# Kernel tuning notes

Hardware: AMD Instinct MI355X
Metric: run time of the kernel (lower is better)

## Reference

```python
import jax, jax.numpy as jnp
import numpy as np

# config (matches init_kwargs)
B, N, C_IN = 2, 16384, 64
NPOINT, NSAMPLE, RADIUS = 2048, 32, 0.8
MLP = [64, 128, 256]
EPS = 1e-5


def _fps(xyz, npoint):
    """Furthest point sampling. xyz: (B,N,3) -> idx (B,npoint) int32."""
    b, n, _ = xyz.shape
    d0 = jnp.sum((xyz - xyz[:, :1, :]) ** 2, -1)  # dist to point 0

    def body(mind, _):
        nxt = jnp.argmax(mind, -1)                       # (B,)
        pt = jnp.take_along_axis(xyz, nxt[:, None, None], 1)  # (B,1,3)
        mind = jnp.minimum(mind, jnp.sum((xyz - pt) ** 2, -1))
        return mind, nxt

    _, idxs = jax.lax.scan(body, d0, None, length=npoint - 1)  # (npoint-1,B)
    idxs = jnp.concatenate([jnp.zeros((1, b), idxs.dtype), idxs], 0)
    return jnp.transpose(idxs).astype(jnp.int32)


def _ball_query(xyz, new_xyz, radius, nsample):
    """First nsample neighbors within radius (pointnet2 semantics: pad with first hit)."""
    n = xyz.shape[1]
    d = jnp.sum((new_xyz[:, :, None, :] - xyz[:, None, :, :]) ** 2, -1)  # (B,np,N)
    mask = d < radius * radius
    # prefer lowest original index among in-range points
    score = jnp.where(mask, -jnp.arange(n, dtype=jnp.float32), -(n + 1.0))
    vals, idxs = jax.lax.top_k(score, nsample)           # (B,np,ns)
    valid = vals > -(n + 0.5)
    idx = jnp.where(valid, idxs, idxs[..., :1])
    cnt = mask.sum(-1)                                    # (B,np)
    return idx.astype(jnp.int32), cnt


def _gather(arr, idx):  # arr (B,N,...), idx (B,...) -> (B,...,...)
    return jax.vmap(lambda a, i: a[i])(arr, idx)


def _bn_eval4(x, g, b):  # (B,C,P,S), eval-mode BN with running mean 0 / var 1
    s = g / jnp.sqrt(1.0 + EPS)
    return x * s[None, :, None, None] + b[None, :, None, None]


def _bn_eval3(x, g, b):  # (B,C,S)
    s = g / jnp.sqrt(1.0 + EPS)
    return x * s[None, :, None] + b[None, :, None]


def setup_inputs() -> dict:
    key = jax.random.key(0)
    ks = jax.random.split(key, 12)
    xyz = jax.random.normal(ks[0], (B, N, 3), jnp.float32)
    features = jax.random.normal(ks[1], (B, C_IN, N), jnp.float32)
    cin = 3 + C_IN
    dims = [cin] + MLP
    inp = {"xyz": xyz, "features": features}
    for li in range(3):
        w = jax.random.normal(ks[2 + li], (dims[li + 1], dims[li]), jnp.float32) / np.sqrt(dims[li])
        inp[f"W{li+1}"] = w
        inp[f"g{li+1}"] = jnp.ones((dims[li + 1],), jnp.float32)
        inp[f"b{li+1}"] = jnp.zeros((dims[li + 1],), jnp.float32)
    npt8, cd, cd8 = NPOINT // 8, MLP[-1], MLP[-1] // 8
    inp["Wq"] = jax.random.normal(ks[5], (npt8, NPOINT), jnp.float32) / np.sqrt(NPOINT)
    inp["gq"] = jnp.ones((npt8,), jnp.float32)
    inp["bq"] = jnp.zeros((npt8,), jnp.float32)
    inp["Wk"] = jax.random.normal(ks[6], (npt8, NPOINT), jnp.float32) / np.sqrt(NPOINT)
    inp["gk"] = jnp.ones((npt8,), jnp.float32)
    inp["bk"] = jnp.zeros((npt8,), jnp.float32)
    inp["We1"] = jax.random.normal(ks[7], (cd8, cd), jnp.float32) / np.sqrt(cd)
    inp["We2"] = jax.random.normal(ks[8], (cd, cd8), jnp.float32) / np.sqrt(cd8)
    inp["alpha"] = jnp.zeros((1,), jnp.float32)  # torch: nn.Parameter(torch.zeros(1))
    return inp


def reference(xyz, features, W1, g1, b1, W2, g2, b2, W3, g3, b3,
              Wq, gq, bq, Wk, gk, bk, We1, We2, alpha):
    # ---- d-FPS sampling (indices are non-differentiable, as in the CUDA op) ----
    xyz_c = jax.lax.stop_gradient(xyz)
    samp = _fps(xyz_c, NPOINT)                       # (B,np)
    new_xyz = _gather(xyz, samp)                     # (B,np,3)
    # ---- ball query + grouping ----
    nn_idx, cnt = _ball_query(xyz_c, jax.lax.stop_gradient(new_xyz), RADIUS, NSAMPLE)
    grouped_xyz = _gather(xyz, nn_idx) - new_xyz[:, :, None, :]        # (B,np,ns,3)
    grouped_feat = _gather(jnp.transpose(features, (0, 2, 1)), nn_idx)  # (B,np,ns,C)
    h = jnp.transpose(jnp.concatenate([grouped_xyz, grouped_feat], -1), (0, 3, 1, 2))  # (B,3+C,np,ns)
    # ---- shared MLP (1x1 conv + BN(eval) + ReLU) ----
    for (w, g, b) in ((W1, g1, b1), (W2, g2, b2), (W3, g3, b3)):
        h = jax.nn.relu(_bn_eval4(jnp.einsum('oi,bips->bops', w, h), g, b))
    h = h * (cnt > 0)[:, None, :, None].astype(h.dtype)  # mask empty balls
    x = jnp.max(h, axis=-1)                               # (B,Cd,np) max-pool over nsample
    # ---- LCEF channel-affinity attention ----
    xh = jnp.transpose(x, (0, 2, 1))                      # (B,np,Cd)
    q = jax.nn.relu(_bn_eval3(jnp.einsum('oi,bis->bos', Wq, xh), gq, bq))  # (B,np/8,Cd)
    k = jax.nn.relu(_bn_eval3(jnp.einsum('oi,bis->bos', Wk, xh), gk, bk))  # (B,np/8,Cd)
    sim = jnp.einsum('bqc,bqd->bcd', k, q)                # (B,Cd,Cd)
    aff = jax.nn.softmax(jnp.max(sim, -1, keepdims=True) - sim, axis=-1)
    s = jnp.max(x, -1)                                    # (B,Cd) squeeze
    e = jax.nn.sigmoid(jnp.einsum('oi,bi->bo', We2, jax.nn.relu(jnp.einsum('oi,bi->bo', We1, s))))
    v = x * e[:, :, None]                                 # excitation
    out = alpha[0] * jnp.einsum('bcd,bdn->bcn', aff, v) + x
    return new_xyz, out
```

## Files before the change

kernel.cpp:

```cpp
#include <hip/hip_runtime.h>
#include <hip/hip_bf16.h>

typedef unsigned short ushort_t;
typedef unsigned int uint_t;
typedef unsigned long long ull_t;

#define B_    2
#define N_    16384
#define NP_   2048
#define NS_   32
#define EPSF  1e-5f

__device__ __forceinline__ float bf2f(ushort_t u) { return __uint_as_float(((uint_t)u) << 16); }

__device__ __forceinline__ int dtflag(const uint_t* g1w) {
  return (g1w[0] == 0x3F803F80u) ? 1 : 0;
}

__device__ __forceinline__ float dist2(float dx, float dy, float dz) {
  return __fadd_rn(__fadd_rn(__fmul_rn(dx, dx), __fmul_rn(dy, dy)), __fmul_rn(dz, dz));
}

template<int CTRL, int RMASK>
__device__ __forceinline__ float dppmax(float x) {
  int m = __builtin_amdgcn_update_dpp(0, __float_as_int(x), CTRL, RMASK, 0xf, true);
  return fmaxf(x, __int_as_float(m));
}
__device__ __forceinline__ float rlanef(float x, int l) {
  return __int_as_float(__builtin_amdgcn_readlane(__float_as_int(x), l));
}

struct CvtTab { const void* src[18]; };
__constant__ int c_psz[18] = {4288, 64, 64, 8192, 128, 128, 32768, 256, 256,
                              524288, 256, 256, 524288, 256, 256, 8192, 8192, 1};
__constant__ int c_poff[18] = {0, 4288, 4352, 4416, 12608, 12736, 12864, 45632, 45888,
                               46144, 570432, 570688, 570944, 1095232, 1095488,
                               1095744, 1103936, 1112128};

__global__ void k_cvt_all(CvtTab tab, float* __restrict__ par) {
  int p = blockIdx.y;
  int n = c_psz[p];
  int i = blockIdx.x * 256 + threadIdx.x;
  if (i >= n) return;
  int f = dtflag((const uint_t*)tab.src[1]);
  float v = f ? bf2f(((const ushort_t*)tab.src[p])[i]) : ((const float*)tab.src[p])[i];
  par[c_poff[p] + i] = v;
}

__global__ void k_wt(const float* __restrict__ W1f, const float* __restrict__ W2f,
                     const float* __restrict__ W3f, float* __restrict__ Wt) {
  int which = blockIdx.y;
  int i = blockIdx.x * 256 + threadIdx.x;
  if (which == 0) {
    if (i >= 4288) return;
    int o = i / 67, k = i - o * 67;
    Wt[k * 64 + o] = W1f[i];
  } else if (which == 1) {
    if (i >= 8192) return;
    int o = i >> 6, k = i & 63;
    Wt[4288 + k * 128 + o] = W2f[i];
  } else {
    if (i >= 32768) return;
    int o = i >> 7, k = i & 127;
    Wt[12480 + k * 256 + o] = W3f[i];
  }
}

__global__ void k_xyz_soa(const void* __restrict__ xyz, const uint_t* __restrict__ g1w,
                          float* __restrict__ X, float* __restrict__ Y, float* __restrict__ Z) {
  int g = blockIdx.x * blockDim.x + threadIdx.x;
  if (g >= B_ * N_) return;
  if (dtflag(g1w)) {
    const ushort_t* p = (const ushort_t*)xyz;
    X[g] = bf2f(p[g * 3 + 0]); Y[g] = bf2f(p[g * 3 + 1]); Z[g] = bf2f(p[g * 3 + 2]);
  } else {
    const float* p = (const float*)xyz;
    X[g] = p[g * 3 + 0]; Y[g] = p[g * 3 + 1]; Z[g] = p[g * 3 + 2];
  }
}

__global__ void k_featT(const void* __restrict__ feat, const uint_t* __restrict__ g1w,
                        float* __restrict__ featF) {
  __shared__ float tile[64 * 65];
  int b = blockIdx.x >> 8, n0 = (blockIdx.x & 255) * 64, t = threadIdx.x;
  int f = dtflag(g1w);
  for (int i = t; i < 4096; i += 256) {
    int c = i >> 6, nn = i & 63;
    size_t src = (size_t)(b * 64 + c) * N_ + n0 + nn;
    tile[c * 65 + nn] = f ? bf2f(((const ushort_t*)feat)[src]) : ((const float*)feat)[src];
  }
  __syncthreads();
  for (int i = t; i < 4096; i += 256) {
    int nn = i >> 6, c = i & 63;
    featF[((size_t)(b * N_ + n0 + nn)) * 64 + c] = tile[c * 65 + nn];
  }
}

__global__ __launch_bounds__(1024)
__attribute__((amdgpu_waves_per_eu(4, 4)))
void k_fps12(const float* __restrict__ X,
             const float* __restrict__ Y,
             const float* __restrict__ Z,
             float* __restrict__ nxf,
             void* __restrict__ outp,
             const uint_t* __restrict__ g1w) {
  __shared__ float sv[16];
  __shared__ float bc[4];
  int b = blockIdx.x, t = threadIdx.x;
  int lane = t & 63, wid = t >> 6;
  int f = dtflag(g1w);
  const float* Xb = X + b * N_;
  const float* Yb = Y + b * N_;
  const float* Zb = Z + b * N_;
  float cx = Xb[0], cy = Yb[0], cz = Zb[0];
  if (t == 0) {
    int base = b * NP_ * 3;
    nxf[base + 0] = cx; nxf[base + 1] = cy; nxf[base + 2] = cz;
    if (f) {
      __hip_bfloat16* o = (__hip_bfloat16*)outp;
      o[base + 0] = __float2bfloat16(cx); o[base + 1] = __float2bfloat16(cy); o[base + 2] = __float2bfloat16(cz);
    } else {
      float* o = (float*)outp;
      o[base + 0] = cx; o[base + 1] = cy; o[base + 2] = cz;
    }
  }
  float x[16], y[16], z[16], md[16];
#pragma unroll
  for (int c = 0; c < 4; c++) {
    float4 xv = ((const float4*)Xb)[(t << 2) + c];
    float4 yv = ((const float4*)Yb)[(t << 2) + c];
    float4 zv = ((const float4*)Zb)[(t << 2) + c];
    x[4 * c + 0] = xv.x; x[4 * c + 1] = xv.y; x[4 * c + 2] = xv.z; x[4 * c + 3] = xv.w;
    y[4 * c + 0] = yv.x; y[4 * c + 1] = yv.y; y[4 * c + 2] = yv.z; y[4 * c + 3] = yv.w;
    z[4 * c + 0] = zv.x; z[4 * c + 1] = zv.y; z[4 * c + 2] = zv.z; z[4 * c + 3] = zv.w;
    md[4 * c + 0] = dist2(xv.x - cx, yv.x - cy, zv.x - cz);
    md[4 * c + 1] = dist2(xv.y - cx, yv.y - cy, zv.y - cz);
    md[4 * c + 2] = dist2(xv.z - cx, yv.z - cy, zv.z - cz);
    md[4 * c + 3] = dist2(xv.w - cx, yv.w - cy, zv.w - cz);
  }
#pragma unroll
  for (int k = 0; k < 16; k++)
    asm volatile("" : "+v"(x[k]), "+v"(y[k]), "+v"(z[k]));

  for (int it = 1; it < NP_; it++) {
    float q0 = fmaxf(fmaxf(md[0], md[1]),   fmaxf(md[2], md[3]));
    float q1 = fmaxf(fmaxf(md[4], md[5]),   fmaxf(md[6], md[7]));
    float q2 = fmaxf(fmaxf(md[8], md[9]),   fmaxf(md[10], md[11]));
    float q3 = fmaxf(fmaxf(md[12], md[13]), fmaxf(md[14], md[15]));
    float lm = fmaxf(fmaxf(q0, q1), fmaxf(q2, q3));
    float v = lm;
    v = dppmax<0x111, 0xf>(v);
    v = dppmax<0x112, 0xf>(v);
    v = dppmax<0x114, 0xf>(v);
    v = dppmax<0x118, 0xf>(v);
    v = dppmax<0x142, 0xa>(v);
    v = dppmax<0x143, 0xc>(v);
    float wm = rlanef(v, 63);
    ull_t m1 = __ballot(lm == wm);
    int wlead = __ffsll((unsigned long long)m1) - 1;
    if (lane == wlead) sv[wid] = wm;
    __syncthreads();
    float pv = sv[lane & 15];
    float q = pv;
    q = dppmax<0x111, 0xf>(q);
    q = dppmax<0x112, 0xf>(q);
    q = dppmax<0x114, 0xf>(q);
    q = dppmax<0x118, 0xf>(q);
    float bm = rlanef(q, 15);
    ull_t m2 = __ballot((lane < 16) && (pv == bm));
    int wwave = __ffsll((unsigned long long)m2) - 1;
    if (wid == wwave && lane == wlead) {
      float wx = x[0], wy = y[0], wz = z[0];
#pragma unroll
      for (int k = 15; k >= 0; k--)
        if (md[k] == lm) { wx = x[k]; wy = y[k]; wz = z[k]; }
      bc[0] = wx; bc[1] = wy; bc[2] = wz;
      int base = (b * NP_ + it) * 3;
      nxf[base + 0] = wx; nxf[base + 1] = wy; nxf[base + 2] = wz;
      if (f) {
        __hip_bfloat16* o = (__hip_bfloat16*)outp;
        o[base + 0] = __float2bfloat16(wx); o[base + 1] = __float2bfloat16(wy); o[base + 2] = __float2bfloat16(wz);
      } else {
        float* o = (float*)outp;
        o[base + 0] = wx; o[base + 1] = wy; o[base + 2] = wz;
      }
    }
    __syncthreads();
    cx = bc[0]; cy = bc[1]; cz = bc[2];
#pragma unroll
    for (int k = 0; k < 16; k++)
      md[k] = fminf(md[k], dist2(x[k] - cx, y[k] - cy, z[k] - cz));
  }
}

__global__ void k_ball(const float* __restrict__ X, const float* __restrict__ Y,
                       const float* __restrict__ Z, const float* __restrict__ nxf,
                       int* __restrict__ nnidx) {
  __shared__ int ibuf[4][NS_];
  int t = threadIdx.x, w = t >> 6, lane = t & 63;
  int cid = blockIdx.x * 4 + w;
  int b = cid >> 11;
  const float* Xb = X + b * N_;
  const float* Yb = Y + b * N_;
  const float* Zb = Z + b * N_;
  float cx = nxf[cid * 3 + 0], cy = nxf[cid * 3 + 1], cz = nxf[cid * 3 + 2];
  int found = 0;
  for (int c = 0; c < N_ / 64; c++) {
    int n = c * 64 + lane;
    float d = dist2(Xb[n] - cx, Yb[n] - cy, Zb[n] - cz);
    bool pred = d < 0.64f;
    ull_t mask = __ballot(pred);
    if (pred) {
      int rank = found + __popcll(mask & ((1ull << lane) - 1ull));
      if (rank < NS_) ibuf[w][rank] = n;
    }
    found += __popcll(mask);
    if (found >= NS_) break;
  }
  __syncthreads();
  if (lane < NS_) {
    int idx = (lane < found) ? ibuf[w][lane] : ibuf[w][0];
    nnidx[cid * NS_ + lane] = idx;
  }
}

__global__ __launch_bounds__(256) void k_mlp(
    const float* __restrict__ featF, const float* __restrict__ X,
    const float* __restrict__ Y, const float* __restrict__ Z,
    const float* __restrict__ nxf, const int* __restrict__ nnidx,
    const float* __restrict__ Wt,
    const float* __restrict__ g1f, const float* __restrict__ b1f,
    const float* __restrict__ g2f, const float* __restrict__ b2f,
    const float* __restrict__ g3f, const float* __restrict__ b3f,
    float* __restrict__ x_nc) {
  __shared__ __align__(16) char smem[33280];
  float* h2f = (float*)smem;
  float* h0f = (float*)(smem + 16384);
  float* h1f = (float*)(smem + 24960);
  int* idxs  = (int*)(smem + 33152);
  const float* Wt1 = Wt;
  const float* Wt2 = Wt + 4288;
  const float* Wt3 = Wt + 12480;

  int t = threadIdx.x;
  int cid = blockIdx.x;
  int b = cid >> 11;
  if (t < 32) idxs[t] = nnidx[cid * NS_ + t];
  __syncthreads();
  float cx = nxf[cid * 3 + 0], cy = nxf[cid * 3 + 1], cz = nxf[cid * 3 + 2];
  if (t < 32) {
    int n = b * N_ + idxs[t];
    h0f[0 * 32 + t] = X[n] - cx;
    h0f[1 * 32 + t] = Y[n] - cy;
    h0f[2 * 32 + t] = Z[n] - cz;
  }
  {
    int s = t >> 3, cg = t & 7;
    const float* fr = featF + ((size_t)(b * N_ + idxs[s])) * 64 + cg * 8;
    float4 a = ((const float4*)fr)[0];
    float4 c2 = ((const float4*)fr)[1];
    int kb = 3 + cg * 8;
    h0f[(kb + 0) * 32 + s] = a.x;  h0f[(kb + 1) * 32 + s] = a.y;
    h0f[(kb + 2) * 32 + s] = a.z;  h0f[(kb + 3) * 32 + s] = a.w;
    h0f[(kb + 4) * 32 + s] = c2.x; h0f[(kb + 5) * 32 + s] = c2.y;
    h0f[(kb + 6) * 32 + s] = c2.z; h0f[(kb + 7) * 32 + s] = c2.w;
  }
  __syncthreads();

  int og = t >> 3, sg = t & 7;
  int s0 = sg * 4;
  {
    int o0 = og * 2;
    float acc[2][4] = {{0, 0, 0, 0}, {0, 0, 0, 0}};
    for (int k = 0; k < 67; k++) {
      float4 h = *(const float4*)(h0f + k * 32 + s0);
      float2 wp = *(const float2*)(Wt1 + k * 64 + o0);
      acc[0][0] = fmaf(wp.x, h.x, acc[0][0]);
      acc[0][1] = fmaf(wp.x, h.y, acc[0][1]);
      acc[0][2] = fmaf(wp.x, h.z, acc[0][2]);
      acc[0][3] = fmaf(wp.x, h.w, acc[0][3]);
      acc[1][0] = fmaf(wp.y, h.x, acc[1][0]);
      acc[1][1] = fmaf(wp.y, h.y, acc[1][1]);
      acc[1][2] = fmaf(wp.y, h.z, acc[1][2]);
      acc[1][3] = fmaf(wp.y, h.w, acc[1][3]);
    }
#pragma unroll
    for (int i2 = 0; i2 < 2; i2++) {
      int o = o0 + i2;
      float sc = g1f[o] / sqrtf(1.0f + EPSF);
      float bb = b1f[o];
      float4 yv;
      yv.x = fmaxf(fmaf(acc[i2][0], sc, bb), 0.0f);
      yv.y = fmaxf(fmaf(acc[i2][1], sc, bb), 0.0f);
      yv.z = fmaxf(fmaf(acc[i2][2], sc, bb), 0.0f);
      yv.w = fmaxf(fmaf(acc[i2][3], sc, bb), 0.0f);
      *(float4*)(h1f + o * 32 + s0) = yv;
    }
  }
  __syncthreads();
  {
    int o0 = og * 4;
    float acc[4][4] = {{0,0,0,0},{0,0,0,0},{0,0,0,0},{0,0,0,0}};
    for (int k = 0; k < 64; k++) {
      float4 h = *(const float4*)(h1f + k * 32 + s0);
      float4 wp = *(const float4*)(Wt2 + k * 128 + o0);
      float w[4] = {wp.x, wp.y, wp.z, wp.w};
#pragma unroll
      for (int i2 = 0; i2 < 4; i2++) {
        acc[i2][0] = fmaf(w[i2], h.x, acc[i2][0]);
        acc[i2][1] = fmaf(w[i2], h.y, acc[i2][1]);
        acc[i2][2] = fmaf(w[i2], h.z, acc[i2][2]);
        acc[i2][3] = fmaf(w[i2], h.w, acc[i2][3]);
      }
    }
#pragma unroll
    for (int i2 = 0; i2 < 4; i2++) {
      int o = o0 + i2;
      float sc = g2f[o] / sqrtf(1.0f + EPSF);
      float bb = b2f[o];
      float4 yv;
      yv.x = fmaxf(fmaf(acc[i2][0], sc, bb), 0.0f);
      yv.y = fmaxf(fmaf(acc[i2][1], sc, bb), 0.0f);
      yv.z = fmaxf(fmaf(acc[i2][2], sc, bb), 0.0f);
      yv.w = fmaxf(fmaf(acc[i2][3], sc, bb), 0.0f);
      *(float4*)(h2f + o * 32 + s0) = yv;
    }
  }
  __syncthreads();
  float acc3[8][4] = {{0,0,0,0},{0,0,0,0},{0,0,0,0},{0,0,0,0},
                      {0,0,0,0},{0,0,0,0},{0,0,0,0},{0,0,0,0}};
  int o0 = og * 8;
  for (int kg = 0; kg < 128; kg++) {
    float4 h = *(const float4*)(h2f + kg * 32 + s0);
    float4 wa = *(const float4*)(Wt3 + kg * 256 + o0);
    float4 wc = *(const float4*)(Wt3 + kg * 256 + o0 + 4);
    float w[8] = {wa.x, wa.y, wa.z, wa.w, wc.x, wc.y, wc.z, wc.w};
#pragma unroll
    for (int i2 = 0; i2 < 8; i2++) {
      acc3[i2][0] = fmaf(w[i2], h.x, acc3[i2][0]);
      acc3[i2][1] = fmaf(w[i2], h.y, acc3[i2][1]);
      acc3[i2][2] = fmaf(w[i2], h.z, acc3[i2][2]);
      acc3[i2][3] = fmaf(w[i2], h.w, acc3[i2][3]);
    }
  }
  float mx[8];
#pragma unroll
  for (int i2 = 0; i2 < 8; i2++) {
    int o = o0 + i2;
    float sc = g3f[o] / sqrtf(1.0f + EPSF);
    float bb = b3f[o];
    float m0 = fmaxf(fmaf(acc3[i2][0], sc, bb), 0.0f);
    float m1 = fmaxf(fmaf(acc3[i2][1], sc, bb), 0.0f);
    float m2 = fmaxf(fmaf(acc3[i2][2], sc, bb), 0.0f);
    float m3 = fmaxf(fmaf(acc3[i2][3], sc, bb), 0.0f);
    mx[i2] = fmaxf(fmaxf(m0, m1), fmaxf(m2, m3));
  }
#pragma unroll
  for (int off = 1; off < 8; off <<= 1) {
#pragma unroll
    for (int i2 = 0; i2 < 8; i2++) mx[i2] = fmaxf(mx[i2], __shfl_xor(mx[i2], off));
  }
  if (sg == 0) {
    float4 a, c;
    a.x = mx[0]; a.y = mx[1]; a.z = mx[2]; a.w = mx[3];
    c.x = mx[4]; c.y = mx[5]; c.z = mx[6]; c.w = mx[7];
    *(float4*)(x_nc + (size_t)cid * 256 + o0) = a;
    *(float4*)(x_nc + (size_t)cid * 256 + o0 + 4) = c;
  }
}

__global__ __launch_bounds__(256) void k_sqmax(const float* __restrict__ x_nc,
                                               float* __restrict__ sqpart) {
  int b = blockIdx.x >> 4, chunk = blockIdx.x & 15, t = threadIdx.x;
  const float* xb = x_nc + (size_t)b * NP_ * 256 + (size_t)chunk * 128 * 256;
  float m = -1e30f;
#pragma unroll 8
  for (int n = 0; n < 128; n++) m = fmaxf(m, xb[(size_t)n * 256 + t]);
  sqpart[(size_t)(b * 16 + chunk) * 256 + t] = m;
}

__global__ __launch_bounds__(256) void k_sqe2(const float* __restrict__ sqpart,
                                              const float* __restrict__ We1f,
                                              const float* __restrict__ We2f,
                                              float* __restrict__ e) {
  __shared__ float ssh[256];
  __shared__ float ush[32];
  int b = blockIdx.x, t = threadIdx.x;
  const float* pp = sqpart + (size_t)b * 16 * 256;
  float m = -1e30f;
#pragma unroll
  for (int c = 0; c < 16; c++) m = fmaxf(m, pp[c * 256 + t]);
  ssh[t] = m;
  __syncthreads();
  if (t < 32) {
    float a = 0.0f;
    for (int i = 0; i < 256; i++) a = fmaf(We1f[t * 256 + i], ssh[i], a);
    ush[t] = fmaxf(a, 0.0f);
  }
  __syncthreads();
  float a = 0.0f;
#pragma unroll
  for (int j = 0; j < 32; j++) a = fmaf(We2f[t * 32 + j], ush[j], a);
  e[b * 256 + t] = 1.0f / (1.0f + expf(-a));
}

__global__ __launch_bounds__(256) void k_qk(const float* __restrict__ x_nc,
                                            const float* __restrict__ Wqf, const float* __restrict__ gqf, const float* __restrict__ bqf,
                                            const float* __restrict__ Wkf, const float* __restrict__ gkf, const float* __restrict__ bkf,
                                            float* __restrict__ qb, float* __restrict__ kb) {
  __shared__ float As[32 * 33];
  __shared__ float Bs[32 * 64];
  int bid = blockIdx.x;
  int b = bid & 1, tq = (bid >> 1) & 1, mt = (bid >> 2) & 7, nt = (bid >> 5) & 3;
  const float* W = tq ? Wkf : Wqf;
  const float* g = tq ? gkf : gqf;
  const float* bb_ = tq ? bkf : bqf;
  float* outp = tq ? kb : qb;
  int t = threadIdx.x;
  int o0 = (t >> 4) * 2, c0 = (t & 15) * 4;
  float acc[2][4] = {{0,0,0,0},{0,0,0,0}};
  for (int k0 = 0; k0 < NP_; k0 += 32) {
    for (int i = t; i < 1024; i += 256) {
      int row = i >> 5, kk = i & 31;
      As[row * 33 + kk] = W[(size_t)(mt * 32 + row) * NP_ + k0 + kk];
    }
    for (int i = t; i < 2048; i += 256) {
      int kk = i >> 6, cc = i & 63;
      Bs[kk * 64 + cc] = x_nc[((size_t)(b * NP_ + k0 + kk)) * 256 + nt * 64 + cc];
    }
    __syncthreads();
    for (int kk = 0; kk < 32; kk++) {
      float4 bv = *(const float4*)(Bs + kk * 64 + c0);
      float a0 = As[(o0 + 0) * 33 + kk];
      float a1 = As[(o0 + 1) * 33 + kk];
      acc[0][0] = fmaf(a0, bv.x, acc[0][0]); acc[0][1] = fmaf(a0, bv.y, acc[0][1]);
      acc[0][2] = fmaf(a0, bv.z, acc[0][2]); acc[0][3] = fmaf(a0, bv.w, acc[0][3]);
      acc[1][0] = fmaf(a1, bv.x, acc[1][0]); acc[1][1] = fmaf(a1, bv.y, acc[1][1]);
      acc[1][2] = fmaf(a1, bv.z, acc[1][2]); acc[1][3] = fmaf(a1, bv.w, acc[1][3]);
    }
    __syncthreads();
  }
#pragma unroll
  for (int i2 = 0; i2 < 2; i2++) {
    int o = mt * 32 + o0 + i2;
    float sc = g[o] / sqrtf(1.0f + EPSF);
    float bv = bb_[o];
    float4 y;
    y.x = fmaxf(fmaf(acc[i2][0], sc, bv), 0.0f);
    y.y = fmaxf(fmaf(acc[i2][1], sc, bv), 0.0f);
    y.z = fmaxf(fmaf(acc[i2][2], sc, bv), 0.0f);
    y.w = fmaxf(fmaf(acc[i2][3], sc, bv), 0.0f);
    *(float4*)(outp + ((size_t)(b * 256 + o)) * 256 + nt * 64 + c0) = y;
  }
}

__global__ __launch_bounds__(256) void k_sim(const float* __restrict__ qb,
                                             const float* __restrict__ kb,
                                             float* __restrict__ sim) {
  __shared__ float As[32 * 64];
  __shared__ float Bs[32 * 64];
  int bid = blockIdx.x;
  int b = bid & 1, ct = (bid >> 1) & 3, dt = (bid >> 3) & 3;
  int t = threadIdx.x;
  int c0 = (t >> 4) * 4, d0 = (t & 15) * 4;
  float acc[4][4] = {{0,0,0,0},{0,0,0,0},{0,0,0,0},{0,0,0,0}};
  for (int k0 = 0; k0 < 256; k0 += 32) {
    for (int i = t; i < 2048; i += 256) {
      int kk = i >> 6, cc = i & 63;
      As[kk * 64 + cc] = kb[((size_t)(b * 256 + k0 + kk)) * 256 + ct * 64 + cc];
      Bs[kk * 64 + cc] = qb[((size_t)(b * 256 + k0 + kk)) * 256 + dt * 64 + cc];
    }
    __syncthreads();
    for (int kk = 0; kk < 32; kk++) {
      float4 av = *(const float4*)(As + kk * 64 + c0);
      float4 bv = *(const float4*)(Bs + kk * 64 + d0);
      acc[0][0] = fmaf(av.x, bv.x, acc[0][0]); acc[0][1] = fmaf(av.x, bv.y, acc[0][1]);
      acc[0][2] = fmaf(av.x, bv.z, acc[0][2]); acc[0][3] = fmaf(av.x, bv.w, acc[0][3]);
      acc[1][0] = fmaf(av.y, bv.x, acc[1][0]); acc[1][1] = fmaf(av.y, bv.y, acc[1][1]);
      acc[1][2] = fmaf(av.y, bv.z, acc[1][2]); acc[1][3] = fmaf(av.y, bv.w, acc[1][3]);
      acc[2][0] = fmaf(av.z, bv.x, acc[2][0]); acc[2][1] = fmaf(av.z, bv.y, acc[2][1]);
      acc[2][2] = fmaf(av.z, bv.z, acc[2][2]); acc[2][3] = fmaf(av.z, bv.w, acc[2][3]);
      acc[3][0] = fmaf(av.w, bv.x, acc[3][0]); acc[3][1] = fmaf(av.w, bv.y, acc[3][1]);
      acc[3][2] = fmaf(av.w, bv.z, acc[3][2]); acc[3][3] = fmaf(av.w, bv.w, acc[3][3]);
    }
    __syncthreads();
  }
#pragma unroll
  for (int i2 = 0; i2 < 4; i2++) {
    *(float4*)(sim + ((size_t)(b * 256 + ct * 64 + c0 + i2)) * 256 + dt * 64 + d0) =
        *(float4*)acc[i2];
  }
}

__global__ void k_aff(const float* __restrict__ sim, float* __restrict__ aff) {
  int t = threadIdx.x, w = t >> 6, lane = t & 63;
  int row = blockIdx.x * 4 + w;
  const float* sr = sim + (size_t)row * 256;
  float4 v = *(const float4*)(sr + lane * 4);
  float mx = fmaxf(fmaxf(v.x, v.y), fmaxf(v.z, v.w));
#pragma unroll
  for (int off = 32; off >= 1; off >>= 1) mx = fmaxf(mx, __shfl_xor(mx, off));
  float4 u;
  u.x = mx - v.x; u.y = mx - v.y; u.z = mx - v.z; u.w = mx - v.w;
  float um = fmaxf(fmaxf(u.x, u.y), fmaxf(u.z, u.w));
#pragma unroll
  for (int off = 32; off >= 1; off >>= 1) um = fmaxf(um, __shfl_xor(um, off));
  float4 p;
  p.x = expf(u.x - um); p.y = expf(u.y - um); p.z = expf(u.z - um); p.w = expf(u.w - um);
  float s = ((p.x + p.y) + (p.z + p.w));
#pragma unroll
  for (int off = 32; off >= 1; off >>= 1) s += __shfl_xor(s, off);
  float4 o;
  o.x = p.x / s; o.y = p.y / s; o.z = p.z / s; o.w = p.w / s;
  *(float4*)(aff + (size_t)row * 256 + lane * 4) = o;
}

__global__ __launch_bounds__(256) void k_out(const float* __restrict__ aff,
                                             const float* __restrict__ x_nc,
                                             const float* __restrict__ e,
                                             const float* __restrict__ alphaf,
                                             void* __restrict__ outp,
                                             const uint_t* __restrict__ g1w) {
  __shared__ float Acs[64 * 33];
  __shared__ float Bs[32 * 65];
  __shared__ float Xs[64 * 65];
  int bid = blockIdx.x;
  int b = bid & 1, ct = (bid >> 1) & 3, nt = bid >> 3;
  int t = threadIdx.x;
  int c0 = (t >> 4) * 4, n0 = (t & 15) * 4;
  float acc[4][4] = {{0,0,0,0},{0,0,0,0},{0,0,0,0},{0,0,0,0}};
  for (int k0 = 0; k0 < 256; k0 += 32) {
    for (int i = t; i < 2048; i += 256) {
      int cc = i >> 5, kk = i & 31;
      Acs[cc * 33 + kk] = aff[((size_t)(b * 256 + ct * 64 + cc)) * 256 + k0 + kk];
    }
    for (int i = t; i < 2048; i += 256) {
      int nn = i >> 5, kk = i & 31;
      Bs[kk * 65 + nn] =
          x_nc[((size_t)(b * NP_ + nt * 64 + nn)) * 256 + k0 + kk] * e[b * 256 + k0 + kk];
    }
    __syncthreads();
    for (int kk = 0; kk < 32; kk++) {
      float a0 = Acs[(c0 + 0) * 33 + kk];
      float a1 = Acs[(c0 + 1) * 33 + kk];
      float a2 = Acs[(c0 + 2) * 33 + kk];
      float a3 = Acs[(c0 + 3) * 33 + kk];
      float b0 = Bs[kk * 65 + n0 + 0];
      float b1 = Bs[kk * 65 + n0 + 1];
      float b2 = Bs[kk * 65 + n0 + 2];
      float b3 = Bs[kk * 65 + n0 + 3];
      acc[0][0] = fmaf(a0, b0, acc[0][0]); acc[0][1] = fmaf(a0, b1, acc[0][1]);
      acc[0][2] = fmaf(a0, b2, acc[0][2]); acc[0][3] = fmaf(a0, b3, acc[0][3]);
      acc[1][0] = fmaf(a1, b0, acc[1][0]); acc[1][1] = fmaf(a1, b1, acc[1][1]);
      acc[1][2] = fmaf(a1, b2, acc[1][2]); acc[1][3] = fmaf(a1, b3, acc[1][3]);
      acc[2][0] = fmaf(a2, b0, acc[2][0]); acc[2][1] = fmaf(a2, b1, acc[2][1]);
      acc[2][2] = fmaf(a2, b2, acc[2][2]); acc[2][3] = fmaf(a2, b3, acc[2][3]);
      acc[3][0] = fmaf(a3, b0, acc[3][0]); acc[3][1] = fmaf(a3, b1, acc[3][1]);
      acc[3][2] = fmaf(a3, b2, acc[3][2]); acc[3][3] = fmaf(a3, b3, acc[3][3]);
    }
    __syncthreads();
  }
  for (int i = t; i < 4096; i += 256) {
    int nn = i >> 6, cc = i & 63;
    Xs[nn * 65 + cc] = x_nc[((size_t)(b * NP_ + nt * 64 + nn)) * 256 + ct * 64 + cc];
  }
  __syncthreads();
  float af = alphaf[0];
  int f = dtflag(g1w);
#pragma unroll
  for (int i2 = 0; i2 < 4; i2++) {
    int c = ct * 64 + c0 + i2;
#pragma unroll
    for (int j = 0; j < 4; j++) {
      float xv = Xs[(n0 + j) * 65 + (c0 + i2)];
      float y = af * acc[i2][j] + xv;
      size_t base = 12288 + ((size_t)(b * 256 + c)) * NP_ + nt * 64 + n0 + j;
      if (f) ((__hip_bfloat16*)outp)[base] = __float2bfloat16(y);
      else   ((float*)outp)[base] = y;
    }
  }
}

extern "C" void kernel_launch(void* const* d_in, const int* in_sizes, int n_in,
                              void* d_out, int out_size, void* d_ws, size_t ws_size,
                              hipStream_t stream) {
  char* ws = (char*)d_ws;
  float* X     = (float*)(ws + 64);
  float* Y     = (float*)(ws + 131136);
  float* Z     = (float*)(ws + 262208);
  float* featF = (float*)(ws + 393280);
  float* par   = (float*)(ws + 8781888);
  float* nxf   = (float*)(ws + 13230464);
  int*   nn    = (int*)(ws + 13279616);
  float* x_nc  = (float*)(ws + 13803904);
  float* qb    = (float*)(ws + 17998208);
  float* kb    = (float*)(ws + 18522496);
  float* sim   = (float*)(ws + 19046784);
  float* aff   = (float*)(ws + 19571072);
  float* evec  = (float*)(ws + 20095360);
  float* Wt    = qb;
  float* sqpart = sim;

  float* W1f = par + 0,      *g1f = par + 4288,    *b1f = par + 4352;
  float* W2f = par + 4416,   *g2f = par + 12608,   *b2f = par + 12736;
  float* W3f = par + 12864,  *g3f = par + 45632,   *b3f = par + 45888;
  float* Wqf = par + 46144,  *gqf = par + 570432,  *bqf = par + 570688;
  float* Wkf = par + 570944, *gkf = par + 1095232, *bkf = par + 1095488;
  float* We1f = par + 1095744, *We2f = par + 1103936, *alphaf = par + 1112128;

  const uint_t* g1w = (const uint_t*)d_in[3];

  CvtTab tab;
  for (int p = 0; p < 18; p++) tab.src[p] = d_in[2 + p];
  k_cvt_all<<<dim3(2048, 18), dim3(256), 0, stream>>>(tab, par);
  k_wt<<<dim3(128, 3), dim3(256), 0, stream>>>(W1f, W2f, W3f, Wt);

  k_xyz_soa<<<dim3(128), dim3(256), 0, stream>>>(d_in[0], g1w, X, Y, Z);
  k_featT<<<dim3(512), dim3(256), 0, stream>>>(d_in[1], g1w, featF);
  k_fps12<<<dim3(2), dim3(1024), 0, stream>>>(X, Y, Z, nxf, d_out, g1w);
  k_ball<<<dim3(1024), dim3(256), 0, stream>>>(X, Y, Z, nxf, nn);
  k_mlp<<<dim3(4096), dim3(256), 0, stream>>>(featF, X, Y, Z, nxf, nn, Wt,
                                              g1f, b1f, g2f, b2f, g3f, b3f, x_nc);
  k_sqmax<<<dim3(32), dim3(256), 0, stream>>>(x_nc, sqpart);
  k_sqe2<<<dim3(2), dim3(256), 0, stream>>>(sqpart, We1f, We2f, evec);
  k_qk<<<dim3(128), dim3(256), 0, stream>>>(x_nc, Wqf, gqf, bqf, Wkf, gkf, bkf, qb, kb);
  k_sim<<<dim3(32), dim3(256), 0, stream>>>(qb, kb, sim);
  k_aff<<<dim3(128), dim3(256), 0, stream>>>(sim, aff);
  k_out<<<dim3(256), dim3(256), 0, stream>>>(aff, x_nc, evec, alphaf, d_out, g1w);
}
```

Baseline: 3.632 ms.

## Merge prep kernels into FPS launch and fuse independent small kernels

Result: no change. 3.572 ms, median of 2 (-1.7%).

```diff
diff --git a/kernel.cpp b/kernel.cpp
--- a/kernel.cpp
+++ b/kernel.cpp
@@ -36,35 +36,8 @@
 __constant__ int c_poff[18] = {0, 4288, 4352, 4416, 12608, 12736, 12864, 45632, 45888,
                                46144, 570432, 570688, 570944, 1095232, 1095488,
                                1095744, 1103936, 1112128};
-
-__global__ void k_cvt_all(CvtTab tab, float* __restrict__ par) {
-  int p = blockIdx.y;
-  int n = c_psz[p];
-  int i = blockIdx.x * 256 + threadIdx.x;
-  if (i >= n) return;
-  int f = dtflag((const uint_t*)tab.src[1]);
-  float v = f ? bf2f(((const ushort_t*)tab.src[p])[i]) : ((const float*)tab.src[p])[i];
-  par[c_poff[p] + i] = v;
-}
-
-__global__ void k_wt(const float* __restrict__ W1f, const float* __restrict__ W2f,
-                     const float* __restrict__ W3f, float* __restrict__ Wt) {
-  int which = blockIdx.y;
-  int i = blockIdx.x * 256 + threadIdx.x;
-  if (which == 0) {
-    if (i >= 4288) return;
-    int o = i / 67, k = i - o * 67;
-    Wt[k * 64 + o] = W1f[i];
-  } else if (which == 1) {
-    if (i >= 8192) return;
-    int o = i >> 6, k = i & 63;
-    Wt[4288 + k * 128 + o] = W2f[i];
-  } else {
-    if (i >= 32768) return;
-    int o = i >> 7, k = i & 127;
-    Wt[12480 + k * 256 + o] = W3f[i];
-  }
-}
+__constant__ int c_pblk[19] = {0, 5, 6, 7, 15, 16, 17, 49, 50, 51, 563, 564, 565,
+                               1077, 1078, 1079, 1087, 1095, 1096};
 
 __global__ void k_xyz_soa(const void* __restrict__ xyz, const uint_t* __restrict__ g1w,
                           float* __restrict__ X, float* __restrict__ Y, float* __restrict__ Z) {
@@ -79,117 +52,163 @@
   }
 }
 
-__global__ void k_featT(const void* __restrict__ feat, const uint_t* __restrict__ g1w,
-                        float* __restrict__ featF) {
-  __shared__ float tile[64 * 65];
-  int b = blockIdx.x >> 8, n0 = (blockIdx.x & 255) * 64, t = threadIdx.x;
-  int f = dtflag(g1w);
-  for (int i = t; i < 4096; i += 256) {
-    int c = i >> 6, nn = i & 63;
-    size_t src = (size_t)(b * 64 + c) * N_ + n0 + nn;
-    tile[c * 65 + nn] = f ? bf2f(((const ushort_t*)feat)[src]) : ((const float*)feat)[src];
-  }
-  __syncthreads();
-  for (int i = t; i < 4096; i += 256) {
-    int nn = i >> 6, c = i & 63;
-    featF[((size_t)(b * N_ + n0 + nn)) * 64 + c] = tile[c * 65 + nn];
-  }
-}
-
 __global__ __launch_bounds__(1024)
 __attribute__((amdgpu_waves_per_eu(4, 4)))
-void k_fps12(const float* __restrict__ X,
-             const float* __restrict__ Y,
-             const float* __restrict__ Z,
-             float* __restrict__ nxf,
-             void* __restrict__ outp,
-             const uint_t* __restrict__ g1w) {
-  __shared__ float sv[16];
-  __shared__ float bc[4];
-  int b = blockIdx.x, t = threadIdx.x;
-  int lane = t & 63, wid = t >> 6;
-  int f = dtflag(g1w);
-  const float* Xb = X + b * N_;
-  const float* Yb = Y + b * N_;
-  const float* Zb = Z + b * N_;
-  float cx = Xb[0], cy = Yb[0], cz = Zb[0];
-  if (t == 0) {
-    int base = b * NP_ * 3;
-    nxf[base + 0] = cx; nxf[base + 1] = cy; nxf[base + 2] = cz;
-    if (f) {
-      __hip_bfloat16* o = (__hip_bfloat16*)outp;
-      o[base + 0] = __float2bfloat16(cx); o[base + 1] = __float2bfloat16(cy); o[base + 2] = __float2bfloat16(cz);
-    } else {
-      float* o = (float*)outp;
-      o[base + 0] = cx; o[base + 1] = cy; o[base + 2] = cz;
-    }
-  }
-  float x[16], y[16], z[16], md[16];
-#pragma unroll
-  for (int c = 0; c < 4; c++) {
-    float4 xv = ((const float4*)Xb)[(t << 2) + c];
-    float4 yv = ((const float4*)Yb)[(t << 2) + c];
-    float4 zv = ((const float4*)Zb)[(t << 2) + c];
-    x[4 * c + 0] = xv.x; x[4 * c + 1] = xv.y; x[4 * c + 2] = xv.z; x[4 * c + 3] = xv.w;
-    y[4 * c + 0] = yv.x; y[4 * c + 1] = yv.y; y[4 * c + 2] = yv.z; y[4 * c + 3] = yv.w;
-    z[4 * c + 0] = zv.x; z[4 * c + 1] = zv.y; z[4 * c + 2] = zv.z; z[4 * c + 3] = zv.w;
-    md[4 * c + 0] = dist2(xv.x - cx, yv.x - cy, zv.x - cz);
-    md[4 * c + 1] = dist2(xv.y - cx, yv.y - cy, zv.y - cz);
-    md[4 * c + 2] = dist2(xv.z - cx, yv.z - cy, zv.z - cz);
-    md[4 * c + 3] = dist2(xv.w - cx, yv.w - cy, zv.w - cz);
-  }
-#pragma unroll
-  for (int k = 0; k < 16; k++)
-    asm volatile("" : "+v"(x[k]), "+v"(y[k]), "+v"(z[k]));
-
-  for (int it = 1; it < NP_; it++) {
-    float q0 = fmaxf(fmaxf(md[0], md[1]),   fmaxf(md[2], md[3]));
-    float q1 = fmaxf(fmaxf(md[4], md[5]),   fmaxf(md[6], md[7]));
-    float q2 = fmaxf(fmaxf(md[8], md[9]),   fmaxf(md[10], md[11]));
-    float q3 = fmaxf(fmaxf(md[12], md[13]), fmaxf(md[14], md[15]));
-    float lm = fmaxf(fmaxf(q0, q1), fmaxf(q2, q3));
-    float v = lm;
-    v = dppmax<0x111, 0xf>(v);
-    v = dppmax<0x112, 0xf>(v);
-    v = dppmax<0x114, 0xf>(v);
-    v = dppmax<0x118, 0xf>(v);
-    v = dppmax<0x142, 0xa>(v);
-    v = dppmax<0x143, 0xc>(v);
-    float wm = rlanef(v, 63);
-    ull_t m1 = __ballot(lm == wm);
-    int wlead = __ffsll((unsigned long long)m1) - 1;
-    if (lane == wlead) sv[wid] = wm;
-    __syncthreads();
-    float pv = sv[lane & 15];
-    float q = pv;
-    q = dppmax<0x111, 0xf>(q);
-    q = dppmax<0x112, 0xf>(q);
-    q = dppmax<0x114, 0xf>(q);
-    q = dppmax<0x118, 0xf>(q);
-    float bm = rlanef(q, 15);
-    ull_t m2 = __ballot((lane < 16) && (pv == bm));
-    int wwave = __ffsll((unsigned long long)m2) - 1;
-    if (wid == wwave && lane == wlead) {
-      float wx = x[0], wy = y[0], wz = z[0];
-#pragma unroll
-      for (int k = 15; k >= 0; k--)
-        if (md[k] == lm) { wx = x[k]; wy = y[k]; wz = z[k]; }
-      bc[0] = wx; bc[1] = wy; bc[2] = wz;
-      int base = (b * NP_ + it) * 3;
-      nxf[base + 0] = wx; nxf[base + 1] = wy; nxf[base + 2] = wz;
+void k_fps_prep(CvtTab tab,
+                const float* __restrict__ X, const float* __restrict__ Y,
+                const float* __restrict__ Z,
+                float* __restrict__ nxf, void* __restrict__ outp,
+                const void* __restrict__ feat,
+                float* __restrict__ par, float* __restrict__ Wt,
+                float* __restrict__ featF) {
+  __shared__ float smem[64 * 65];
+  int bid = blockIdx.x, t = threadIdx.x;
+  const uint_t* g1w = (const uint_t*)tab.src[1];
+
+  if (bid < 2) {
+    float* sv = smem;
+    float* bc = smem + 16;
+    int b = bid;
+    int lane = t & 63, wid = t >> 6;
+    int f = dtflag(g1w);
+    const float* Xb = X + b * N_;
+    const float* Yb = Y + b * N_;
+    const float* Zb = Z + b * N_;
+    float cx = Xb[0], cy = Yb[0], cz = Zb[0];
+    if (t == 0) {
+      int base = b * NP_ * 3;
+      nxf[base + 0] = cx; nxf[base + 1] = cy; nxf[base + 2] = cz;
       if (f) {
         __hip_bfloat16* o = (__hip_bfloat16*)outp;
-        o[base + 0] = __float2bfloat16(wx); o[base + 1] = __float2bfloat16(wy); o[base + 2] = __float2bfloat16(wz);
+        o[base + 0] = __float2bfloat16(cx); o[base + 1] = __float2bfloat16(cy); o[base + 2] = __float2bfloat16(cz);
       } else {
         float* o = (float*)outp;
-        o[base + 0] = wx; o[base + 1] = wy; o[base + 2] = wz;
+        o[base + 0] = cx; o[base + 1] = cy; o[base + 2] = cz;
       }
     }
-    __syncthreads();
-    cx = bc[0]; cy = bc[1]; cz = bc[2];
+    float x[16], y[16], z[16], md[16];
+#pragma unroll
+    for (int c = 0; c < 4; c++) {
+      float4 xv = ((const float4*)Xb)[(t << 2) + c];
+      float4 yv = ((const float4*)Yb)[(t << 2) + c];
+      float4 zv = ((const float4*)Zb)[(t << 2) + c];
+      x[4 * c + 0] = xv.x; x[4 * c + 1] = xv.y; x[4 * c + 2] = xv.z; x[4 * c + 3] = xv.w;
+      y[4 * c + 0] = yv.x; y[4 * c + 1] = yv.y; y[4 * c + 2] = yv.z; y[4 * c + 3] = yv.w;
+      z[4 * c + 0] = zv.x; z[4 * c + 1] = zv.y; z[4 * c + 2] = zv.z; z[4 * c + 3] = zv.w;
+      md[4 * c + 0] = dist2(xv.x - cx, yv.x - cy, zv.x - cz);
+      md[4 * c + 1] = dist2(xv.y - cx, yv.y - cy, zv.y - cz);
+      md[4 * c + 2] = dist2(xv.z - cx, yv.z - cy, zv.z - cz);
+      md[4 * c + 3] = dist2(xv.w - cx, yv.w - cy, zv.w - cz);
+    }
 #pragma unroll
     for (int k = 0; k < 16; k++)
-      md[k] = fminf(md[k], dist2(x[k] - cx, y[k] - cy, z[k] - cz));
+      asm volatile("" : "+v"(x[k]), "+v"(y[k]), "+v"(z[k]));
+
+    for (int it = 1; it < NP_; it++) {
+      float q0 = fmaxf(fmaxf(md[0], md[1]),   fmaxf(md[2], md[3]));
+      float q1 = fmaxf(fmaxf(md[4], md[5]),   fmaxf(md[6], md[7]));
+      float q2 = fmaxf(fmaxf(md[8], md[9]),   fmaxf(md[10], md[11]));
+      float q3 = fmaxf(fmaxf(md[12], md[13]), fmaxf(md[14], md[15]));
+      float lm = fmaxf(fmaxf(q0, q1), fmaxf(q2, q3));
+      float v = lm;
+      v = dppmax<0x111, 0xf>(v);
+      v = dppmax<0x112, 0xf>(v);
+      v = dppmax<0x114, 0xf>(v);
+      v = dppmax<0x118, 0xf>(v);
+      v = dppmax<0x142, 0xa>(v);
+      v = dppmax<0x143, 0xc>(v);
+      float wm = rlanef(v, 63);
+      ull_t m1 = __ballot(lm == wm);
+      int wlead = __ffsll((unsigned long long)m1) - 1;
+      if (lane == wlead) sv[wid] = wm;
+      __syncthreads();
+      float pv = sv[lane & 15];
+      float q = pv;
+      q = dppmax<0x111, 0xf>(q);
+      q = dppmax<0x112, 0xf>(q);
+      q = dppmax<0x114, 0xf>(q);
+      q = dppmax<0x118, 0xf>(q);
+      float bm = rlanef(q, 15);
+      ull_t m2 = __ballot((lane < 16) && (pv == bm));
+      int wwave = __ffsll((unsigned long long)m2) - 1;
+      if (wid == wwave && lane == wlead) {
+        float wx = x[0], wy = y[0], wz = z[0];
+#pragma unroll
+        for (int k = 15; k >= 0; k--)
+          if (md[k] == lm) { wx = x[k]; wy = y[k]; wz = z[k]; }
+        bc[0] = wx; bc[1] = wy; bc[2] = wz;
+        int base = (b * NP_ + it) * 3;
+        nxf[base + 0] = wx; nxf[base + 1] = wy; nxf[base + 2] = wz;
+        if (f) {
+          __hip_bfloat16* o = (__hip_bfloat16*)outp;
+          o[base + 0] = __float2bfloat16(wx); o[base + 1] = __float2bfloat16(wy); o[base + 2] = __float2bfloat16(wz);
+        } else {
+          float* o = (float*)outp;
+          o[base + 0] = wx; o[base + 1] = wy; o[base + 2] = wz;
+        }
+      }
+      __syncthreads();
+      cx = bc[0]; cy = bc[1]; cz = bc[2];
+#pragma unroll
+      for (int k = 0; k < 16; k++)
+        md[k] = fminf(md[k], dist2(x[k] - cx, y[k] - cy, z[k] - cz));
+    }
+    return;
+  }
+
+  int f = dtflag(g1w);
+  if (bid < 514) {
+    int tile_id = bid - 2;
+    int b = tile_id >> 8, n0 = (tile_id & 255) * 64;
+    for (int i = t; i < 4096; i += 1024) {
+      int c = i >> 6, nn = i & 63;
+      size_t src = (size_t)(b * 64 + c) * N_ + n0 + nn;
+      smem[c * 65 + nn] = f ? bf2f(((const ushort_t*)feat)[src]) : ((const float*)feat)[src];
+    }
+    __syncthreads();
+    for (int i = t; i < 4096; i += 1024) {
+      int nn = i >> 6, c = i & 63;
+      featF[((size_t)(b * N_ + n0 + nn)) * 64 + c] = smem[c * 65 + nn];
+    }
+    return;
+  }
+  if (bid < 559) {
+    int wi = bid - 514;
+    if (wi < 5) {
+      int i = wi * 1024 + t;
+      if (i < 4288) {
+        float v = f ? bf2f(((const ushort_t*)tab.src[0])[i]) : ((const float*)tab.src[0])[i];
+        int o = i / 67, k = i - o * 67;
+        Wt[k * 64 + o] = v;
+      }
+    } else if (wi < 13) {
+      int i = (wi - 5) * 1024 + t;
+      if (i < 8192) {
+        float v = f ? bf2f(((const ushort_t*)tab.src[3])[i]) : ((const float*)tab.src[3])[i];
+        int o = i >> 6, k = i & 63;
+        Wt[4288 + k * 128 + o] = v;
+      }
+    } else {
+      int i = (wi - 13) * 1024 + t;
+      if (i < 32768) {
+        float v = f ? bf2f(((const ushort_t*)tab.src[6])[i]) : ((const float*)tab.src[6])[i];
+        int o = i >> 7, k = i & 127;
+        Wt[12480 + k * 256 + o] = v;
+      }
+    }
+    return;
+  }
+  {
+    int blk = bid - 559;
+    int p = 0;
+#pragma unroll
+    for (int q = 0; q < 18; q++)
+      if (blk >= c_pblk[q + 1]) p = q + 1;
+    int i = (blk - c_pblk[p]) * 1024 + t;
+    if (i < c_psz[p]) {
+      float v = f ? bf2f(((const ushort_t*)tab.src[p])[i]) : ((const float*)tab.src[p])[i];
+      par[c_poff[p] + i] = v;
+    }
   }
 }
 
@@ -369,54 +388,29 @@
   }
 }
 
-__global__ __launch_bounds__(256) void k_sqmax(const float* __restrict__ x_nc,
-                                               float* __restrict__ sqpart) {
-  int b = blockIdx.x >> 4, chunk = blockIdx.x & 15, t = threadIdx.x;
-  const float* xb = x_nc + (size_t)b * NP_ * 256 + (size_t)chunk * 128 * 256;
-  float m = -1e30f;
-#pragma unroll 8
-  for (int n = 0; n < 128; n++) m = fmaxf(m, xb[(size_t)n * 256 + t]);
-  sqpart[(size_t)(b * 16 + chunk) * 256 + t] = m;
-}
-
-__global__ __launch_bounds__(256) void k_sqe2(const float* __restrict__ sqpart,
-                                              const float* __restrict__ We1f,
-                                              const float* __restrict__ We2f,
-                                              float* __restrict__ e) {
-  __shared__ float ssh[256];
-  __shared__ float ush[32];
-  int b = blockIdx.x, t = threadIdx.x;
-  const float* pp = sqpart + (size_t)b * 16 * 256;
-  float m = -1e30f;
-#pragma unroll
-  for (int c = 0; c < 16; c++) m = fmaxf(m, pp[c * 256 + t]);
-  ssh[t] = m;
-  __syncthreads();
-  if (t < 32) {
-    float a = 0.0f;
-    for (int i = 0; i < 256; i++) a = fmaf(We1f[t * 256 + i], ssh[i], a);
-    ush[t] = fmaxf(a, 0.0f);
-  }
-  __syncthreads();
-  float a = 0.0f;
-#pragma unroll
-  for (int j = 0; j < 32; j++) a = fmaf(We2f[t * 32 + j], ush[j], a);
-  e[b * 256 + t] = 1.0f / (1.0f + expf(-a));
-}
-
-__global__ __launch_bounds__(256) void k_qk(const float* __restrict__ x_nc,
-                                            const float* __restrict__ Wqf, const float* __restrict__ gqf, const float* __restrict__ bqf,
-                                            const float* __restrict__ Wkf, const float* __restrict__ gkf, const float* __restrict__ bkf,
-                                            float* __restrict__ qb, float* __restrict__ kb) {
+__global__ __launch_bounds__(256) void k_sqmax_qk(
+    const float* __restrict__ x_nc, float* __restrict__ sqpart,
+    const float* __restrict__ Wqf, const float* __restrict__ gqf, const float* __restrict__ bqf,
+    const float* __restrict__ Wkf, const float* __restrict__ gkf, const float* __restrict__ bkf,
+    float* __restrict__ qb, float* __restrict__ kb) {
   __shared__ float As[32 * 33];
   __shared__ float Bs[32 * 64];
-  int bid = blockIdx.x;
+  int bigid = blockIdx.x, t = threadIdx.x;
+  if (bigid < 32) {
+    int b = bigid >> 4, chunk = bigid & 15;
+    const float* xb = x_nc + (size_t)b * NP_ * 256 + (size_t)chunk * 128 * 256;
+    float m = -1e30f;
+#pragma unroll 8
+    for (int n = 0; n < 128; n++) m = fmaxf(m, xb[(size_t)n * 256 + t]);
+    sqpart[(size_t)(b * 16 + chunk) * 256 + t] = m;
+    return;
+  }
+  int bid = bigid - 32;
   int b = bid & 1, tq = (bid >> 1) & 1, mt = (bid >> 2) & 7, nt = (bid >> 5) & 3;
   const float* W = tq ? Wkf : Wqf;
   const float* g = tq ? gkf : gqf;
   const float* bb_ = tq ? bkf : bqf;
   float* outp = tq ? kb : qb;
-  int t = threadIdx.x;
   int o0 = (t >> 4) * 2, c0 = (t & 15) * 4;
   float acc[2][4] = {{0,0,0,0},{0,0,0,0}};
   for (int k0 = 0; k0 < NP_; k0 += 32) {
@@ -454,14 +448,39 @@
   }
 }
 
-__global__ __launch_bounds__(256) void k_sim(const float* __restrict__ qb,
-                                             const float* __restrict__ kb,
-                                             float* __restrict__ sim) {
+__global__ __launch_bounds__(256) void k_sqe_sim(
+    const float* __restrict__ sqpart,
+    const float* __restrict__ We1f, const float* __restrict__ We2f,
+    float* __restrict__ e,
+    const float* __restrict__ qb, const float* __restrict__ kb,
+    float* __restrict__ sim) {
   __shared__ float As[32 * 64];
   __shared__ float Bs[32 * 64];
-  int bid = blockIdx.x;
+  int bigid = blockIdx.x, t = threadIdx.x;
+  if (bigid < 2) {
+    float* ssh = As;
+    float* ush = As + 256;
+    int b = bigid;
+    const float* pp = sqpart + (size_t)b * 16 * 256;
+    float m = -1e30f;
+#pragma unroll
+    for (int c = 0; c < 16; c++) m = fmaxf(m, pp[c * 256 + t]);
+    ssh[t] = m;
+    __syncthreads();
+    if (t < 32) {
+      float a = 0.0f;
+      for (int i = 0; i < 256; i++) a = fmaf(We1f[t * 256 + i], ssh[i], a);
+      ush[t] = fmaxf(a, 0.0f);
+    }
+    __syncthreads();
+    float a = 0.0f;
+#pragma unroll
+    for (int j = 0; j < 32; j++) a = fmaf(We2f[t * 32 + j], ush[j], a);
+    e[b * 256 + t] = 1.0f / (1.0f + expf(-a));
+    return;
+  }
+  int bid = bigid - 2;
   int b = bid & 1, ct = (bid >> 1) & 3, dt = (bid >> 3) & 3;
-  int t = threadIdx.x;
   int c0 = (t >> 4) * 4, d0 = (t & 15) * 4;
   float acc[4][4] = {{0,0,0,0},{0,0,0,0},{0,0,0,0},{0,0,0,0}};
   for (int k0 = 0; k0 < 256; k0 += 32) {
@@ -599,32 +618,29 @@
   float* aff   = (float*)(ws + 19571072);
   float* evec  = (float*)(ws + 20095360);
   float* Wt    = qb;
-  float* sqpart = sim;
-
-  float* W1f = par + 0,      *g1f = par + 4288,    *b1f = par + 4352;
-  float* W2f = par + 4416,   *g2f = par + 12608,   *b2f = par + 12736;
-  float* W3f = par + 12864,  *g3f = par + 45632,   *b3f = par + 45888;
-  float* Wqf = par + 46144,  *gqf = par + 570432,  *bqf = par + 570688;
-  float* Wkf = par + 570944, *gkf = par + 1095232, *bkf = par + 1095488;
+  float* sqpart = aff;
+
+  float* g1f = par + 4288,    *b1f = par + 4352;
+  float* g2f = par + 12608,   *b2f = par + 12736;
+  float* g3f = par + 45632,   *b3f = par + 45888;
+  float* Wqf = par + 46144,   *gqf = par + 570432,  *bqf = par + 570688;
+  float* Wkf = par + 570944,  *gkf = par + 1095232, *bkf = par + 1095488;
   float* We1f = par + 1095744, *We2f = par + 1103936, *alphaf = par + 1112128;
 
   const uint_t* g1w = (const uint_t*)d_in[3];
 
   CvtTab tab;
   for (int p = 0; p < 18; p++) tab.src[p] = d_in[2 + p];
-  k_cvt_all<<<dim3(2048, 18), dim3(256), 0, stream>>>(tab, par);
-  k_wt<<<dim3(128, 3), dim3(256), 0, stream>>>(W1f, W2f, W3f, Wt);
 
   k_xyz_soa<<<dim3(128), dim3(256), 0, stream>>>(d_in[0], g1w, X, Y, Z);
-  k_featT<<<dim3(512), dim3(256), 0, stream>>>(d_in[1], g1w, featF);
-  k_fps12<<<dim3(2), dim3(1024), 0, stream>>>(X, Y, Z, nxf, d_out, g1w);
+  k_fps_prep<<<dim3(1655), dim3(1024), 0, stream>>>(tab, X, Y, Z, nxf, d_out,
+                                                    d_in[1], par, Wt, featF);
   k_ball<<<dim3(1024), dim3(256), 0, stream>>>(X, Y, Z, nxf, nn);
   k_mlp<<<dim3(4096), dim3(256), 0, stream>>>(featF, X, Y, Z, nxf, nn, Wt,
                                               g1f, b1f, g2f, b2f, g3f, b3f, x_nc);
-  k_sqmax<<<dim3(32), dim3(256), 0, stream>>>(x_nc, sqpart);
-  k_sqe2<<<dim3(2), dim3(256), 0, stream>>>(sqpart, We1f, We2f, evec);
-  k_qk<<<dim3(128), dim3(256), 0, stream>>>(x_nc, Wqf, gqf, bqf, Wkf, gkf, bkf, qb, kb);
-  k_sim<<<dim3(32), dim3(256), 0, stream>>>(qb, kb, sim);
+  k_sqmax_qk<<<dim3(160), dim3(256), 0, stream>>>(x_nc, sqpart,
+                                                  Wqf, gqf, bqf, Wkf, gkf, bkf, qb, kb);
+  k_sqe_sim<<<dim3(34), dim3(256), 0, stream>>>(sqpart, We1f, We2f, evec, qb, kb, sim);
   k_aff<<<dim3(128), dim3(256), 0, stream>>>(sim, aff);
   k_out<<<dim3(256), dim3(256), 0, stream>>>(aff, x_nc, evec, alphaf, d_out, g1w);
 }
```
